# Performance work log

Measured on AMD Instinct MI355X. Metric: run time of the kernel, lower is better.

## Reference

```python
import jax, jax.numpy as jnp
import numpy as np

EPS = 1e-5

def setup_inputs() -> dict:
    key = jax.random.key(0)
    k1, k2, k3 = jax.random.split(key, 3)
    B, D, T = 16, 512, 1024
    K = 8192
    x = jax.random.normal(k1, (B, D, T), dtype=jnp.float32)
    embedding_sum = jax.random.normal(k2, (K, D), dtype=jnp.float32)
    cluster_usage = jax.random.uniform(k3, (K,), dtype=jnp.float32)
    return {"x": x, "embedding_sum": embedding_sum, "cluster_usage": cluster_usage}

def reference(x, embedding_sum, cluster_usage):
    # embedding = embedding_sum / clamp(cluster_usage, eps)  -> [K, D]
    emb = embedding_sum / jnp.clip(cluster_usage, EPS, None)[:, None]
    B, D, T = x.shape
    # encode: [B, D, T] -> [B*T, D]
    xf = jnp.transpose(x, (0, 2, 1)).reshape(B * T, D)
    # squared Euclidean distance (argmin-equivalent to cdist p=2)
    x2 = jnp.sum(xf * xf, axis=1, keepdims=True)          # [N, 1]
    e2 = jnp.sum(emb * emb, axis=1)                        # [K]
    d2 = x2 - 2.0 * (xf @ emb.T) + e2[None, :]             # [N, K]
    codes = jnp.argmin(d2, axis=-1).reshape(B, 1, T)       # [B, 1, T]
    # decode: gather codebook vectors
    quantized = emb[codes[:, 0, :]]                        # [B, T, D]
    quantized = jnp.transpose(quantized, (0, 2, 1))        # [B, D, T]
    return codes, quantized
```

## Files before the change

### kernel.cpp

```cpp
#include <hip/hip_runtime.h>
#include <hip/hip_bf16.h>
#include <cfloat>
#include <stdint.h>

#define EPS 1e-5f
constexpr int Dd = 512, Tt = 1024, Kk = 8192;
constexpr int Nq = 16 * 1024;
constexpr float TAU = 1.5f;

typedef __bf16 bf16x8 __attribute__((ext_vector_type(8)));
typedef float  f32x4  __attribute__((ext_vector_type(4)));
typedef unsigned long long u64;

union Pack8 { __bf16 h[8]; int4 v; };

__device__ __forceinline__ void gld16(const void* g, void* l) {
    __builtin_amdgcn_global_load_lds(
        (const __attribute__((address_space(1))) uint32_t*)g,
        (__attribute__((address_space(3))) uint32_t*)l, 16, 0, 0);
}

__device__ __forceinline__ unsigned monokey(float s) {
    unsigned b = __float_as_uint(s);
    return b ^ ((unsigned)((int)b >> 31) | 0x80000000u);
}
__device__ __forceinline__ float unmono(unsigned u) {
    u = (u & 0x80000000u) ? (u ^ 0x80000000u) : ~u;
    return __uint_as_float(u);
}

__device__ __forceinline__ void merge2u(unsigned& a1, unsigned& a2, unsigned b1, unsigned b2) {
    unsigned c1 = min(a1, b1);
    unsigned c2 = min(max(a1, b1), min(a2, b2));
    a1 = c1; a2 = c2;
}
__device__ __forceinline__ u64 umin64(u64 a, u64 b) { return a < b ? a : b; }
__device__ __forceinline__ u64 umax64(u64 a, u64 b) { return a > b ? a : b; }
__device__ __forceinline__ void merge4q(u64& a1, u64& a2, u64& a3, u64& a4,
                                        u64 b1, u64 b2, u64 b3, u64 b4) {
    u64 c1 = umin64(a1, b1);
    u64 c2 = umin64(umin64(a2, b2), umax64(a1, b1));
    u64 c3 = umin64(umin64(a3, b3), umin64(umax64(a2, b1), umax64(a1, b2)));
    u64 c4 = umin64(umin64(a4, b4), umin64(umax64(a3, b1), umax64(a1, b3)));
    c4 = umin64(c4, umax64(a2, b2));
    a1 = c1; a2 = c2; a3 = c3; a4 = c4;
}
__device__ __forceinline__ u64 shflx64(u64 v, int m) {
    int lo = __shfl_xor((int)(unsigned)v, m, 64);
    int hi = __shfl_xor((int)(v >> 32), m, 64);
    return ((u64)(unsigned)hi << 32) | (unsigned)lo;
}

__global__ __launch_bounds__(256) void split_x_kernel(const float* __restrict__ x,
                                                      ushort* __restrict__ Xh,
                                                      float* __restrict__ Xf,
                                                      int* __restrict__ cnt) {
    if (blockIdx.x == 0 && threadIdx.x < 2) cnt[threadIdx.x] = 0;
    __shared__ float Ls[64][68];
    const int tid = threadIdx.x, bid = blockIdx.x;
    const int b  = bid >> 7;
    const int d0 = ((bid >> 4) & 7) * 64;
    const int t0 = (bid & 15) * 64;
    const float* xb = x + ((size_t)b * Dd + d0) * Tt + t0;
#pragma unroll
    for (int it = 0; it < 4; ++it) {
        int s = it * 256 + tid;
        int d = s >> 4, c = (s & 15) * 4;
        float4 g = *(const float4*)(xb + (size_t)d * Tt + c);
        *(float4*)&Ls[d][c] = g;
    }
    __syncthreads();
    const int t = tid >> 2;
    const int dseg = (tid & 3) * 16;
    Pack8 ph[2];
    float vf[16];
#pragma unroll
    for (int dd = 0; dd < 16; ++dd) {
        float v = Ls[dseg + dd][t];
        vf[dd] = v;
        ph[dd >> 3].h[dd & 7] = (__bf16)v;
    }
    size_t base = ((size_t)(b * Tt + t0 + t)) * Dd + d0 + dseg;
    *(int4*)(Xh + base)     = ph[0].v;
    *(int4*)(Xh + base + 8) = ph[1].v;
#pragma unroll
    for (int g = 0; g < 4; ++g)
        *(float4*)(Xf + base + g * 4) = make_float4(vf[g*4], vf[g*4+1], vf[g*4+2], vf[g*4+3]);
}

__global__ __launch_bounds__(256) void split_e_kernel(const float* __restrict__ es,
                                                      const float* __restrict__ usage,
                                                      ushort* __restrict__ Eh,
                                                      float* __restrict__ embf,
                                                      double* __restrict__ e2d,
                                                      float* __restrict__ e2f) {
    const int wave = threadIdx.x >> 6, lane = threadIdx.x & 63;
    const int k = blockIdx.x * 4 + wave;
    const float uc = fmaxf(usage[k], EPS);
    const float* row = es + (size_t)k * Dd;
    const int d = lane * 8;
    float4 a = *(const float4*)(row + d);
    float4 c = *(const float4*)(row + d + 4);
    float ef[8] = {a.x/uc, a.y/uc, a.z/uc, a.w/uc, c.x/uc, c.y/uc, c.z/uc, c.w/uc};
    Pack8 ph;
    double e2 = 0.0;
#pragma unroll
    for (int j = 0; j < 8; ++j) {
        ph.h[j] = (__bf16)ef[j];
        e2 = fma((double)ef[j], (double)ef[j], e2);
    }
    size_t base = (size_t)k * Dd + d;
    *(int4*)(Eh + base) = ph.v;
    *(float4*)(embf + base)     = make_float4(ef[0], ef[1], ef[2], ef[3]);
    *(float4*)(embf + base + 4) = make_float4(ef[4], ef[5], ef[6], ef[7]);
#pragma unroll
    for (int off = 32; off >= 1; off >>= 1) e2 += __shfl_down(e2, off, 64);
    if (lane == 0) { e2d[k] = e2; e2f[k] = (float)e2; }
}

__device__ __forceinline__ void stageA2(const ushort* __restrict__ Xh, char* buf,
                                        int m0, int d0, int tid, int j0) {
#pragma unroll
    for (int j = 0; j < 2; ++j) {
        int s = (j0 + j) * 512 + tid;
        int row = s >> 3;
        int clog = (s & 7) ^ (row & 7);
        gld16(Xh + (size_t)(m0 + row) * Dd + d0 + clog * 8, buf + s * 16);
    }
}
__device__ __forceinline__ void stageB2(const ushort* __restrict__ Eh, char* buf,
                                        int n0, int d0, int tid, int j0) {
#pragma unroll
    for (int j = 0; j < 2; ++j) {
        int s = (j0 + j) * 512 + tid;
        int row = s >> 3;
        int clog = (s & 7) ^ (row & 7);
        gld16(Eh + (size_t)(n0 + row) * Dd + d0 + clog * 8, buf + 32768 + s * 16);
    }
}

#define SB() __builtin_amdgcn_sched_barrier(0)

__global__ __launch_bounds__(512) void gemm_kernel(const ushort* __restrict__ Xh,
                                                   const ushort* __restrict__ Eh,
                                                   const float* __restrict__ e2f,
                                                   uint2* __restrict__ colres) {
    __shared__ int4 ldsbuf[8192];
    char* lds = (char*)ldsbuf;

    const int tid = threadIdx.x;
    int wg = blockIdx.x;
    int wgid = (wg & 7) * 256 + (wg >> 3);
    int st = wgid >> 5, u = wgid & 31;
    int mb = (st >> 3) * 8 + (u & 7);
    int nb = (st & 7) * 4 + (u >> 3);
    const int m0 = mb * 256, n0 = nb * 256;

    const int wave = tid >> 6, lane = tid & 63;
    const int wm = wave >> 1, wn = wave & 1;
    const int mw = wm * 64, nw = wn * 128;
    const int fm = lane & 15, fq = lane >> 4;
    const int fm7 = fm & 7;
    const int x0 = (fq ^ fm7) * 16;
    const int x1 = ((4 + fq) ^ fm7) * 16;
    const int pao = (mw + fm) * 128;
    const int pbo = 32768 + (nw + fm) * 128;

    f32x4 acc[8][4] = {};
    bf16x8 a0[4], a1[4], bl0[4], bh0[4], bl1[4], bh1[4];

    stageA2(Xh, lds, m0, 0, tid, 0);
    stageA2(Xh, lds, m0, 0, tid, 2);
    stageB2(Eh, lds, n0, 0, tid, 0);
    stageB2(Eh, lds, n0, 0, tid, 2);
    stageA2(Xh, lds + 65536, m0, 64, tid, 0);
    asm volatile("s_waitcnt vmcnt(2)" ::: "memory");
    __builtin_amdgcn_s_barrier();
    SB();
#pragma unroll
    for (int i = 0; i < 4; ++i) a0[i]  = *(const bf16x8*)(lds + pao + i * 2048 + x0);
#pragma unroll
    for (int i = 0; i < 4; ++i) bl0[i] = *(const bf16x8*)(lds + pbo + i * 2048 + x0);
    SB();

    for (int t = 0; t < 8; ++t) {
        char* bufc = lds + (t & 1) * 65536;
        char* bufn = lds + ((t + 1) & 1) * 65536;
        const char* pA = bufc + pao;
        const char* pB = bufc + pbo;
        const int d1 = (t + 1) * 64, d2 = (t + 2) * 64;

#pragma unroll
        for (int i = 0; i < 4; ++i) bh0[i] = *(const bf16x8*)(pB + 8192 + i * 2048 + x0);
        SB();
        if (t + 1 < 8) stageA2(Xh, bufn, m0, d1, tid, 2);
        SB();
        asm volatile("s_waitcnt lgkmcnt(4)" ::: "memory");
        SB();
        __builtin_amdgcn_s_setprio(1);
#pragma unroll
        for (int i = 0; i < 4; ++i)
#pragma unroll
            for (int j = 0; j < 4; ++j)
                acc[i][j] = __builtin_amdgcn_mfma_f32_16x16x32_bf16(bl0[i], a0[j], acc[i][j], 0, 0, 0);
        __builtin_amdgcn_s_setprio(0);
        SB();
        __builtin_amdgcn_s_barrier();

#pragma unroll
        for (int i = 0; i < 4; ++i) a1[i]  = *(const bf16x8*)(pA + i * 2048 + x1);
#pragma unroll
        for (int i = 0; i < 4; ++i) bl1[i] = *(const bf16x8*)(pB + i * 2048 + x1);
        SB();
        if (t + 1 < 8) stageB2(Eh, bufn, n0, d1, tid, 0);
        SB();
        asm volatile("s_waitcnt lgkmcnt(8)" ::: "memory");
        SB();
        __builtin_amdgcn_s_setprio(1);
#pragma unroll
        for (int i = 0; i < 4; ++i)
#pragma unroll
            for (int j = 0; j < 4; ++j)
                acc[i + 4][j] = __builtin_amdgcn_mfma_f32_16x16x32_bf16(bh0[i], a0[j], acc[i + 4][j], 0, 0, 0);
        __builtin_amdgcn_s_setprio(0);
        SB();
        __builtin_amdgcn_s_barrier();

#pragma unroll
        for (int i = 0; i < 4; ++i) bh1[i] = *(const bf16x8*)(pB + 8192 + i * 2048 + x1);
        SB();
        if (t + 1 < 8) stageB2(Eh, bufn, n0, d1, tid, 2);
        SB();
        asm volatile("s_waitcnt lgkmcnt(4)" ::: "memory");
        SB();
        __builtin_amdgcn_s_setprio(1);
#pragma unroll
        for (int i = 0; i < 4; ++i)
#pragma unroll
            for (int j = 0; j < 4; ++j)
                acc[i][j] = __builtin_amdgcn_mfma_f32_16x16x32_bf16(bl1[i], a1[j], acc[i][j], 0, 0, 0);
        __builtin_amdgcn_s_setprio(0);
        SB();
        __builtin_amdgcn_s_barrier();

        asm volatile("s_waitcnt lgkmcnt(0)" ::: "memory");
        SB();
        __builtin_amdgcn_s_barrier();
        if (t + 2 < 8) stageA2(Xh, bufc, m0, d2, tid, 0);
        SB();
        __builtin_amdgcn_s_setprio(1);
#pragma unroll
        for (int i = 0; i < 4; ++i)
#pragma unroll
            for (int j = 0; j < 4; ++j)
                acc[i + 4][j] = __builtin_amdgcn_mfma_f32_16x16x32_bf16(bh1[i], a1[j], acc[i + 4][j], 0, 0, 0);
        __builtin_amdgcn_s_setprio(0);
        SB();

        if (t < 7) {
            if (t < 6) { asm volatile("s_waitcnt vmcnt(2)" ::: "memory"); }
            else       { asm volatile("s_waitcnt vmcnt(0)" ::: "memory"); }
            SB();
            __builtin_amdgcn_s_barrier();
            SB();
            const char* pAn = bufn + pao;
            const char* pBn = bufn + pbo;
#pragma unroll
            for (int i = 0; i < 4; ++i) a0[i]  = *(const bf16x8*)(pAn + i * 2048 + x0);
#pragma unroll
            for (int i = 0; i < 4; ++i) bl0[i] = *(const bf16x8*)(pBn + i * 2048 + x0);
            SB();
        }
    }

    float4 e2v[8];
#pragma unroll
    for (int ni = 0; ni < 8; ++ni)
        e2v[ni] = *(const float4*)(e2f + n0 + nw + ni * 16 + fq * 4);

    const int cb = (n0 + nw) >> 7;
#pragma unroll
    for (int mj = 0; mj < 4; ++mj) {
        unsigned s1 = 0xFFFFFFFFu, s2 = 0xFFFFFFFFu;
#pragma unroll
        for (int ni = 0; ni < 8; ++ni) {
            unsigned k0 = (monokey(fmaf(-2.0f, acc[ni][mj][0], e2v[ni].x)) & 0xFFFFFF80u) | (unsigned)(ni * 16 + fq * 4 + 0);
            unsigned k1 = (monokey(fmaf(-2.0f, acc[ni][mj][1], e2v[ni].y)) & 0xFFFFFF80u) | (unsigned)(ni * 16 + fq * 4 + 1);
            unsigned k2 = (monokey(fmaf(-2.0f, acc[ni][mj][2], e2v[ni].z)) & 0xFFFFFF80u) | (unsigned)(ni * 16 + fq * 4 + 2);
            unsigned k3 = (monokey(fmaf(-2.0f, acc[ni][mj][3], e2v[ni].w)) & 0xFFFFFF80u) | (unsigned)(ni * 16 + fq * 4 + 3);
            unsigned lo01 = min(k0, k1), hi01 = max(k0, k1);
            unsigned lo23 = min(k2, k3), hi23 = max(k2, k3);
            unsigned p1 = min(lo01, lo23);
            unsigned p2 = min(max(lo01, lo23), min(hi01, hi23));
            merge2u(s1, s2, p1, p2);
        }
#pragma unroll
        for (int stg = 16; stg <= 32; stg <<= 1) {
            unsigned b1 = __shfl_xor(s1, stg, 64);
            unsigned b2 = __shfl_xor(s2, stg, 64);
            merge2u(s1, s2, b1, b2);
        }
        if (lane < 16)
            colres[(size_t)(m0 + mw + mj * 16 + lane) * 64 + cb] = make_uint2(s1, s2);
    }
}

__global__ __launch_bounds__(256) void merge_kernel(const uint2* __restrict__ colres,
                                                    float* __restrict__ out,
                                                    int* __restrict__ cnt,
                                                    int* __restrict__ queueC,
                                                    int* __restrict__ queueF) {
    const int wave = threadIdx.x >> 6, lane = threadIdx.x & 63;
    const int row = blockIdx.x * 4 + wave;
    uint2 q = colres[(size_t)row * 64 + lane];
    const unsigned nb128 = (unsigned)(lane * 128);
    u64 a1 = ((u64)(q.x & 0xFFFFFF80u) << 32) | (nb128 + (q.x & 127u));
    u64 a2 = ((u64)(q.y & 0xFFFFFF80u) << 32) | (nb128 + (q.y & 127u));
    u64 a3 = ~0ull, a4 = ~0ull;
#pragma unroll
    for (int st = 1; st < 64; st <<= 1)
        merge4q(a1, a2, a3, a4, shflx64(a1, st), shflx64(a2, st), shflx64(a3, st), shflx64(a4, st));
    float v1 = unmono((unsigned)(a1 >> 32));
    u64 coll = __ballot(unmono(q.y) < v1 + TAU);
    if (lane == 0) {
        float v2 = unmono((unsigned)(a2 >> 32));
        float v4 = unmono((unsigned)(a4 >> 32));
        int i1 = (int)(unsigned)a1;
        out[row] = (float)i1;
        if (coll != 0ull || (v4 - v1 < TAU)) {
            int p = atomicAdd(&cnt[1], 1);
            queueF[p] = row;
        } else if (v2 - v1 < TAU) {
            int p = atomicAdd(&cnt[0], 1);
            queueC[p * 5]     = row;
            queueC[p * 5 + 1] = i1;
            queueC[p * 5 + 2] = (int)(unsigned)a2;
            queueC[p * 5 + 3] = (int)(unsigned)a3;
            queueC[p * 5 + 4] = (int)(unsigned)a4;
        }
    }
}

__global__ __launch_bounds__(256) void cand_kernel(const float* __restrict__ Xf,
                                                   const float* __restrict__ embf,
                                                   const double* __restrict__ e2d,
                                                   const int* __restrict__ cnt,
                                                   const int* __restrict__ queueC,
                                                   float* __restrict__ out) {
    const int wv = (blockIdx.x << 2) | (threadIdx.x >> 6);
    const int lane = threadIdx.x & 63;
    const int n = cnt[0];
    for (int p = wv; p < n; p += gridDim.x * 4) {
        int row = queueC[p * 5];
        int ci[4] = {queueC[p*5+1], queueC[p*5+2], queueC[p*5+3], queueC[p*5+4]};
        const float* xr = Xf + (size_t)row * Dd + lane * 8;
        float4 xa = *(const float4*)xr;
        float4 xb = *(const float4*)(xr + 4);
        double s[4] = {0.0, 0.0, 0.0, 0.0};
#pragma unroll
        for (int c = 0; c < 4; ++c) {
            const float* er = embf + (size_t)ci[c] * Dd + lane * 8;
            float4 ea = *(const float4*)er;
            float4 eb = *(const float4*)(er + 4);
            double t = 0.0;
            t = fma((double)xa.x, (double)ea.x, t);
            t = fma((double)xa.y, (double)ea.y, t);
            t = fma((double)xa.z, (double)ea.z, t);
            t = fma((double)xa.w, (double)ea.w, t);
            t = fma((double)xb.x, (double)eb.x, t);
            t = fma((double)xb.y, (double)eb.y, t);
            t = fma((double)xb.z, (double)eb.z, t);
            t = fma((double)xb.w, (double)eb.w, t);
            s[c] = t;
        }
#pragma unroll
        for (int off = 32; off >= 1; off >>= 1) {
#pragma unroll
            for (int c = 0; c < 4; ++c) s[c] += __shfl_down(s[c], off, 64);
        }
        if (lane == 0) {
            double bv = DBL_MAX; int bi = 0x7fffffff;
#pragma unroll
            for (int c = 0; c < 4; ++c) {
                double dv = fma(-2.0, s[c], e2d[ci[c]]);
                if (dv < bv || (dv == bv && ci[c] < bi)) { bv = dv; bi = ci[c]; }
            }
            out[row] = (float)bi;
        }
    }
}

__global__ __launch_bounds__(256) void fscan_kernel(const float* __restrict__ Xf,
                                                    const float* __restrict__ embf,
                                                    const double* __restrict__ e2d,
                                                    const int* __restrict__ cnt,
                                                    const int* __restrict__ queueF,
                                                    double* __restrict__ fbv,
                                                    int* __restrict__ fbi) {
    __shared__ float xs[512];
    __shared__ double sv[256];
    __shared__ int si[256];
    const int tid = threadIdx.x;
    const int ntask = cnt[1] * 16;
    for (int task = blockIdx.x; task < ntask; task += gridDim.x) {
        int qi = task >> 4, ch = task & 15;
        int row = queueF[qi];
        __syncthreads();
        for (int d = tid; d < Dd; d += 256)
            xs[d] = Xf[(size_t)row * Dd + d];
        __syncthreads();
        double bv = DBL_MAX; int bi = 0x7fffffff;
#pragma unroll
        for (int c = 0; c < 2; ++c) {
            int k = ch * 512 + c * 256 + tid;
            const float* er = embf + (size_t)k * Dd;
            double a0 = 0, a1 = 0, a2 = 0, a3 = 0;
            for (int d = 0; d < Dd; d += 4) {
                float4 e = *(const float4*)(er + d);
                float4 xv = *(const float4*)&xs[d];
                a0 = fma((double)e.x, (double)xv.x, a0);
                a1 = fma((double)e.y, (double)xv.y, a1);
                a2 = fma((double)e.z, (double)xv.z, a2);
                a3 = fma((double)e.w, (double)xv.w, a3);
            }
            double s = fma(-2.0, (a0 + a1) + (a2 + a3), e2d[k]);
            if (s < bv || (s == bv && k < bi)) { bv = s; bi = k; }
        }
        sv[tid] = bv; si[tid] = bi;
        __syncthreads();
        for (int off = 128; off > 0; off >>= 1) {
            if (tid < off) {
                if (sv[tid + off] < sv[tid] ||
                    (sv[tid + off] == sv[tid] && si[tid + off] < si[tid])) {
                    sv[tid] = sv[tid + off]; si[tid] = si[tid + off];
                }
            }
            __syncthreads();
        }
        if (tid == 0) { fbv[task] = sv[0]; fbi[task] = si[0]; }
    }
}

__global__ void fmerge_kernel(const int* __restrict__ cnt,
                              const int* __restrict__ queueF,
                              const double* __restrict__ fbv,
                              const int* __restrict__ fbi,
                              float* __restrict__ out) {
    const int nF = cnt[1];
    for (int qi = blockIdx.x * 256 + threadIdx.x; qi < nF; qi += gridDim.x * 256) {
        double bv = DBL_MAX; int bi = 0x7fffffff;
        for (int c = 0; c < 16; ++c) {
            double v = fbv[qi * 16 + c]; int i = fbi[qi * 16 + c];
            if (v < bv || (v == bv && i < bi)) { bv = v; bi = i; }
        }
        out[queueF[qi]] = (float)bi;
    }
}

__global__ __launch_bounds__(256) void gather_kernel(const float* __restrict__ embf,
                                                     float* __restrict__ out) {
    __shared__ int cs[64];
    const int tid = threadIdx.x;
    const int m0 = blockIdx.x * 64;
    const int b = m0 >> 10;
    const int t0 = m0 & (Tt - 1);
    if (tid < 64) cs[tid] = (int)out[m0 + tid];
    __syncthreads();
    const int tq = tid & 63;
    const int dg = tid >> 6;
    const int c = cs[tq];
    const float* row = embf + (size_t)c * Dd;
    float* ob = out + Nq + (size_t)b * Dd * Tt + t0 + tq;
#pragma unroll 4
    for (int d = dg * 128; d < dg * 128 + 128; ++d)
        ob[(size_t)d * Tt] = row[d];
}

extern "C" void kernel_launch(void* const* d_in, const int* in_sizes, int n_in,
                              void* d_out, int out_size, void* d_ws, size_t ws_size,
                              hipStream_t stream) {
    const float* x     = (const float*)d_in[0];
    const float* es    = (const float*)d_in[1];
    const float* usage = (const float*)d_in[2];
    float* out = (float*)d_out;

    char* w = (char*)d_ws;
    ushort* Xh = (ushort*)w;   w += (size_t)Nq * Dd * 2;
    ushort* Eh = (ushort*)w;   w += (size_t)Kk * Dd * 2;
    float*  Xf = (float*)w;    w += (size_t)Nq * Dd * 4;
    float*  embf = (float*)w;  w += (size_t)Kk * Dd * 4;
    double* e2d = (double*)w;  w += (size_t)Kk * 8;
    float*  e2f = (float*)w;   w += (size_t)Kk * 4;
    uint2* colres = (uint2*)w; w += (size_t)Nq * 64 * 8;
    int* cnt = (int*)w;        w += 256;
    int* queueC = (int*)w;     w += (size_t)Nq * 5 * 4;
    int* queueF = (int*)w;     w += (size_t)Nq * 4;
    double* fbv = (double*)Xh;
    int*    fbi = (int*)((char*)Xh + 4 * 1024 * 1024);

    split_x_kernel<<<2048, 256, 0, stream>>>(x, Xh, Xf, cnt);
    split_e_kernel<<<Kk / 4, 256, 0, stream>>>(es, usage, Eh, embf, e2d, e2f);
    gemm_kernel<<<2048, 512, 0, stream>>>(Xh, Eh, e2f, colres);
    merge_kernel<<<Nq / 4, 256, 0, stream>>>(colres, out, cnt, queueC, queueF);
    cand_kernel<<<256, 256, 0, stream>>>(Xf, embf, e2d, cnt, queueC, out);
    fscan_kernel<<<256, 256, 0, stream>>>(Xf, embf, e2d, cnt, queueF, fbv, fbi);
    fmerge_kernel<<<64, 256, 0, stream>>>(cnt, queueF, fbv, fbi, out);
    gather_kernel<<<Nq / 64, 256, 0, stream>>>(embf, out);
}
```

Before: 371.6 us.

## Batch eight fallback queries per block in fp64 rescan kernel

The fp64 fallback scan now handles eight queued rows per task instead of one, so each codebook row loaded from global memory is reused across eight query vectors held in padded shared memory. The block-wide shared-memory tree reduction is replaced with wavefront shuffle reductions followed by a small cross-wave merge. This cuts codebook memory traffic for the fallback path, at the cost of eight fp64 accumulators per thread (more register pressure) and padded duplicate work when the queue size is not a multiple of eight.

Result: slower. 395.4 us (+6.4%).

```diff
diff --git a/kernel.cpp b/kernel.cpp
--- a/kernel.cpp
+++ b/kernel.cpp
@@ -397,47 +397,77 @@
                                                     const int* __restrict__ queueF,
                                                     double* __restrict__ fbv,
                                                     int* __restrict__ fbi) {
-    __shared__ float xs[512];
-    __shared__ double sv[256];
-    __shared__ int si[256];
+    __shared__ float xs[8][516];
+    __shared__ double svw[8][4];
+    __shared__ int    siw[8][4];
     const int tid = threadIdx.x;
-    const int ntask = cnt[1] * 16;
+    const int nF = cnt[1];
+    const int nqb = (nF + 7) >> 3;
+    const int ntask = nqb * 16;
     for (int task = blockIdx.x; task < ntask; task += gridDim.x) {
-        int qi = task >> 4, ch = task & 15;
-        int row = queueF[qi];
+        const int qb = task >> 4, ch = task & 15;
         __syncthreads();
-        for (int d = tid; d < Dd; d += 256)
-            xs[d] = Xf[(size_t)row * Dd + d];
+        {
+            int qq  = tid >> 5;
+            int seg = tid & 31;
+            int qi = qb * 8 + qq; if (qi >= nF) qi = nF - 1;
+            int row = queueF[qi];
+            const float* xr = Xf + (size_t)row * Dd + seg * 16;
+            float* dst = &xs[qq][seg * 16];
+            *(float4*)(dst)      = *(const float4*)(xr);
+            *(float4*)(dst + 4)  = *(const float4*)(xr + 4);
+            *(float4*)(dst + 8)  = *(const float4*)(xr + 8);
+            *(float4*)(dst + 12) = *(const float4*)(xr + 12);
+        }
         __syncthreads();
-        double bv = DBL_MAX; int bi = 0x7fffffff;
+        double bv[8]; int bi[8];
+#pragma unroll
+        for (int q = 0; q < 8; ++q) { bv[q] = DBL_MAX; bi[q] = 0x7fffffff; }
 #pragma unroll
         for (int c = 0; c < 2; ++c) {
             int k = ch * 512 + c * 256 + tid;
             const float* er = embf + (size_t)k * Dd;
-            double a0 = 0, a1 = 0, a2 = 0, a3 = 0;
+            double acc[8] = {};
             for (int d = 0; d < Dd; d += 4) {
                 float4 e = *(const float4*)(er + d);
-                float4 xv = *(const float4*)&xs[d];
-                a0 = fma((double)e.x, (double)xv.x, a0);
-                a1 = fma((double)e.y, (double)xv.y, a1);
-                a2 = fma((double)e.z, (double)xv.z, a2);
-                a3 = fma((double)e.w, (double)xv.w, a3);
-            }
-            double s = fma(-2.0, (a0 + a1) + (a2 + a3), e2d[k]);
-            if (s < bv || (s == bv && k < bi)) { bv = s; bi = k; }
-        }
-        sv[tid] = bv; si[tid] = bi;
-        __syncthreads();
-        for (int off = 128; off > 0; off >>= 1) {
-            if (tid < off) {
-                if (sv[tid + off] < sv[tid] ||
-                    (sv[tid + off] == sv[tid] && si[tid + off] < si[tid])) {
-                    sv[tid] = sv[tid + off]; si[tid] = si[tid + off];
+#pragma unroll
+                for (int q = 0; q < 8; ++q) {
+                    float4 xv = *(const float4*)&xs[q][d];
+                    acc[q] = fma((double)e.x, (double)xv.x, acc[q]);
+                    acc[q] = fma((double)e.y, (double)xv.y, acc[q]);
+                    acc[q] = fma((double)e.z, (double)xv.z, acc[q]);
+                    acc[q] = fma((double)e.w, (double)xv.w, acc[q]);
                 }
             }
-            __syncthreads();
-        }
-        if (tid == 0) { fbv[task] = sv[0]; fbi[task] = si[0]; }
+            double e2k = e2d[k];
+#pragma unroll
+            for (int q = 0; q < 8; ++q) {
+                double s = fma(-2.0, acc[q], e2k);
+                if (s < bv[q] || (s == bv[q] && k < bi[q])) { bv[q] = s; bi[q] = k; }
+            }
+        }
+        const int lane = tid & 63, wvi = tid >> 6;
+#pragma unroll
+        for (int q = 0; q < 8; ++q) {
+#pragma unroll
+            for (int off = 32; off >= 1; off >>= 1) {
+                double vb = __shfl_down(bv[q], off, 64);
+                int    ib = __shfl_down(bi[q], off, 64);
+                if (vb < bv[q] || (vb == bv[q] && ib < bi[q])) { bv[q] = vb; bi[q] = ib; }
+            }
+            if (lane == 0) { svw[q][wvi] = bv[q]; siw[q][wvi] = bi[q]; }
+        }
+        __syncthreads();
+        if (tid < 8) {
+            double b = svw[tid][0]; int i = siw[tid][0];
+#pragma unroll
+            for (int w = 1; w < 4; ++w)
+                if (svw[tid][w] < b || (svw[tid][w] == b && siw[tid][w] < i)) {
+                    b = svw[tid][w]; i = siw[tid][w];
+                }
+            int qi = qb * 8 + tid;
+            if (qi < nF) { fbv[(size_t)qi * 16 + ch] = b; fbi[(size_t)qi * 16 + ch] = i; }
+        }
     }
 }
 
```
